# Kernel optimization log

Measured on AMD Instinct MI355X. Metric: run time of the kernel, lower is better.

Reference implementation:

```python
import jax, jax.numpy as jnp
import numpy as np

GAMMA = 0.002


def setup_inputs() -> dict:
    key = jax.random.key(0)
    k1, k2, k3, k4 = jax.random.split(key, 4)
    n, m, d = 16384, 8192, 512
    X = jax.random.normal(k1, (n, d), dtype=jnp.float32)
    Y = jax.random.normal(k2, (m, d), dtype=jnp.float32)
    # nn.Linear(m, 1): weight (1, m), bias (1,), default torch init ~ U(-1/sqrt(m), 1/sqrt(m))
    bound = 1.0 / np.sqrt(m)
    W = jax.random.uniform(k3, (1, m), dtype=jnp.float32, minval=-bound, maxval=bound)
    b = jax.random.uniform(k4, (1,), dtype=jnp.float32, minval=-bound, maxval=bound)
    return {"X": X, "Y": Y, "W": W, "b": b}


def reference(X, Y, W, b):
    # RBF Gram matrix via the GEMM squared-distance trick:
    x2 = jnp.sum(X * X, axis=-1, keepdims=True)          # (n, 1)
    y2 = jnp.sum(Y * Y, axis=-1)[None, :]                # (1, m)
    xy = jnp.einsum('nd,md->nm', X, Y)                   # (n, m)
    sq = jnp.maximum(x2 + y2 - 2.0 * xy, 0.0)            # clamp tiny negatives
    K = jnp.exp(-GAMMA * sq)                             # (n, m)
    # Linear(m -> 1) then squeeze(-1)
    out = jnp.einsum('nm,om->no', K, W) + b              # (n, 1)
    return out[:, 0]
```

## Files before the change

kernel.cpp:

```cpp
#include <hip/hip_runtime.h>
#include <hip/hip_bf16.h>


#define GAMMA 0.002f

typedef __bf16 bf16x8 __attribute__((ext_vector_type(8)));
typedef float  f32x4  __attribute__((ext_vector_type(4)));
typedef __attribute__((address_space(3))) void lds_void_t;
typedef __attribute__((address_space(1))) const void gl_void_t;

__global__ __launch_bounds__(256) void prep_x(const float* __restrict__ src,
                                              __bf16* __restrict__ dst,
                                              float* __restrict__ fac) {
    const int wid  = threadIdx.x >> 6;
    const int lane = threadIdx.x & 63;
    const int row  = blockIdx.x * 4 + wid;
    const float4* s = reinterpret_cast<const float4*>(src + (size_t)row * 512);
    float4 v0 = s[lane * 2];
    float4 v1 = s[lane * 2 + 1];
    float acc = v0.x * v0.x + v0.y * v0.y + v0.z * v0.z + v0.w * v0.w
              + v1.x * v1.x + v1.y * v1.y + v1.z * v1.z + v1.w * v1.w;
    bf16x8 o;
    o[0] = (__bf16)v0.x; o[1] = (__bf16)v0.y; o[2] = (__bf16)v0.z; o[3] = (__bf16)v0.w;
    o[4] = (__bf16)v1.x; o[5] = (__bf16)v1.y; o[6] = (__bf16)v1.z; o[7] = (__bf16)v1.w;
    *reinterpret_cast<bf16x8*>(dst + (size_t)row * 512 + lane * 8) = o;
#pragma unroll
    for (int off = 32; off >= 1; off >>= 1) acc += __shfl_xor(acc, off, 64);
    if (lane == 0) fac[row] = __expf(-GAMMA * acc);
}

__global__ __launch_bounds__(256) void prep_y(const float* __restrict__ src,
                                              __bf16* __restrict__ dst,
                                              float* __restrict__ fac,
                                              const float* __restrict__ W) {
    const int wid  = threadIdx.x >> 6;
    const int lane = threadIdx.x & 63;
    const int m    = blockIdx.x * 4 + wid;
    const float4* s = reinterpret_cast<const float4*>(src + (size_t)m * 512);
    float4 v0 = s[lane * 2];
    float4 v1 = s[lane * 2 + 1];
    float acc = v0.x * v0.x + v0.y * v0.y + v0.z * v0.z + v0.w * v0.w
              + v1.x * v1.x + v1.y * v1.y + v1.z * v1.z + v1.w * v1.w;
    bf16x8 o;
    o[0] = (__bf16)v0.x; o[1] = (__bf16)v0.y; o[2] = (__bf16)v0.z; o[3] = (__bf16)v0.w;
    o[4] = (__bf16)v1.x; o[5] = (__bf16)v1.y; o[6] = (__bf16)v1.z; o[7] = (__bf16)v1.w;
    const size_t idx = ((size_t)(lane >> 2) * 512 + (m >> 4)) * 512
                     + ((lane & 3) * 16 + (m & 15)) * 8;
    *reinterpret_cast<bf16x8*>(dst + idx) = o;
#pragma unroll
    for (int off = 32; off >= 1; off >>= 1) acc += __shfl_xor(acc, off, 64);
    if (lane == 0) fac[m] = __expf(-GAMMA * acc) * W[m];
}

__global__ void init_out(float* __restrict__ out, const float* __restrict__ b, int n) {
    int i = blockIdx.x * blockDim.x + threadIdx.x;
    if (i < n) out[i] = b[0];
}


#define LOADB(B, C) do { \
    const int q_ = (C) & 15, p_ = (C) >> 4; \
    const __bf16* bp_ = Ybt + ((size_t)q_ * 512 + cbgBase + p_ * 32) * 512 + lane8; \
    B[0] = *reinterpret_cast<const bf16x8*>(bp_); \
    B[1] = *reinterpret_cast<const bf16x8*>(bp_ + 512); \
    B[2] = *reinterpret_cast<const bf16x8*>(bp_ + 1024); \
    B[3] = *reinterpret_cast<const bf16x8*>(bp_ + 1536); \
} while (0)

#define READA(A, Q) do { \
    _Pragma("unroll") \
    for (int rb = 0; rb < 4; ++rb) \
        A[rb] = *reinterpret_cast<const bf16x8*>( \
            &smem[(Q) * 4096 + rb * 1024 + lane16]); \
} while (0)

#define MFMA16(A, B) do { \
    __builtin_amdgcn_s_setprio(1); \
    _Pragma("unroll") \
    for (int rb = 0; rb < 4; ++rb) \
        _Pragma("unroll") \
        for (int cb = 0; cb < 4; ++cb) \
            acc[rb][cb] = __builtin_amdgcn_mfma_f32_16x16x32_bf16( \
                A[rb], B[cb], acc[rb][cb], 0, 0, 0); \
    __builtin_amdgcn_s_setprio(0); \
} while (0)

__global__ __launch_bounds__(512, 4) void rbf_gemm(
    const __bf16* __restrict__ Xb, const __bf16* __restrict__ Ybt,
    const float* __restrict__ ex, const float* __restrict__ cwp,
    float* __restrict__ out) {
    __shared__ __align__(128) char smem[81920];

    const int tid  = threadIdx.x;
    const int wid  = tid >> 6;
    const int lane = tid & 63;

    const int pid = blockIdx.x;
    const int xcd = pid & 7;
    const int j   = pid >> 3;
    const int ch  = xcd & 1;
    const int rg  = (xcd >> 1) * 64 + j;
    const int rowBase = rg * 64;
    const int colBase = ch * 4096;
    const int cbgBase = ch * 256 + wid * 4;

    const int l15 = lane & 15, l4 = lane >> 4;
    const int lane16 = lane * 16;
    const int lane8  = lane * 8;

#pragma unroll
    for (int i = 0; i < 8; ++i) {
        const int blk = wid * 8 + i;
        const int q = blk >> 2, rb = blk & 3;
        const __bf16* src = Xb + (size_t)(rowBase + rb * 16 + l15) * 512 + q * 32 + l4 * 8;
        __builtin_amdgcn_global_load_lds((gl_void_t*)src,
            (lds_void_t*)(smem + q * 4096 + rb * 1024), 16, 0, 0);
    }
#pragma unroll
    for (int i = 0; i < 2; ++i)
        __builtin_amdgcn_global_load_lds(
            (gl_void_t*)(cwp + colBase + wid * 512 + i * 256 + lane * 4),
            (lds_void_t*)(smem + 65536 + wid * 2048 + i * 1024), 16, 0, 0);
    asm volatile("s_waitcnt vmcnt(0)");
    __builtin_amdgcn_s_barrier();

    f32x4 acc[4][4] = {};
    float rowsum[4][4] = {};

    bf16x8 A0[4], A1[4], B0[4], B1[4];
    LOADB(B0, 0);

    for (int cc = 0; cc < 64; ++cc) {
        const int ce = 2 * cc, co = 2 * cc + 1;
        LOADB(B1, co);
        READA(A0, ce & 15);
        MFMA16(A0, B0);
        LOADB(B0, (co + 1) & 127);
        READA(A1, co & 15);
        MFMA16(A1, B1);
        if ((cc & 7) == 7) {
            const int p = cc >> 3;
            float cv[4];
#pragma unroll
            for (int cb = 0; cb < 4; ++cb)
                cv[cb] = *reinterpret_cast<const float*>(
                    &smem[65536 + (p * 512 + wid * 64 + cb * 16 + l15) * 4]);
#pragma unroll
            for (int rb = 0; rb < 4; ++rb)
#pragma unroll
                for (int i2 = 0; i2 < 4; ++i2) {
                    float s = rowsum[rb][i2];
#pragma unroll
                    for (int cb = 0; cb < 4; ++cb)
                        s += __expf(0.004f * acc[rb][cb][i2]) * cv[cb];
                    rowsum[rb][i2] = s;
                }
#pragma unroll
            for (int rb = 0; rb < 4; ++rb)
#pragma unroll
                for (int cb = 0; cb < 4; ++cb)
                    acc[rb][cb] = (f32x4){0.f, 0.f, 0.f, 0.f};
        }
    }

#pragma unroll
    for (int rb = 0; rb < 4; ++rb)
#pragma unroll
        for (int i2 = 0; i2 < 4; ++i2) {
            float s = rowsum[rb][i2];
#pragma unroll
            for (int off = 1; off < 16; off <<= 1) s += __shfl_xor(s, off, 64);
            if (l15 == 0) {
                const int n = rowBase + rb * 16 + l4 * 4 + i2;
                atomicAdd(&out[n], ex[n] * s);
            }
        }
}

extern "C" void kernel_launch(void* const* d_in, const int* in_sizes, int n_in,
                              void* d_out, int out_size, void* d_ws, size_t ws_size,
                              hipStream_t stream) {
    const float* X = (const float*)d_in[0];
    const float* Y = (const float*)d_in[1];
    const float* W = (const float*)d_in[2];
    const float* b = (const float*)d_in[3];
    float* out = (float*)d_out;

    char* ws = (char*)d_ws;
    __bf16* Xb  = (__bf16*)(ws);
    __bf16* Ybt = (__bf16*)(ws + 16777216);
    float*  ex  = (float*)(ws + 16777216 + 8388608);
    float*  cw  = (float*)(ws + 16777216 + 8388608 + 65536);

    prep_x<<<4096, 256, 0, stream>>>(X, Xb, ex);
    prep_y<<<2048, 256, 0, stream>>>(Y, Ybt, cw, W);
    init_out<<<64, 256, 0, stream>>>(out, b, 16384);
    rbf_gemm<<<512, 512, 0, stream>>>(Xb, Ybt, ex, cw, out);
}
```

Measured before the change: 152.4 us.

## Fold output init into prep_x and drop B register double-buffering

The separate init_out launch is removed and the bias is written to out from prep_x's lane 0, saving one kernel launch. The GEMM main loop's manual double-buffered B loads (load the next chunk while computing the current one) are replaced by a single-buffer loop that loads B, reads A and then issues the MFMAs. This cuts register pressure but exposes global-load latency unless the compiler reschedules the loads, so the loop may stall more.

Result: faster. 145.4 us (-4.6%).

```diff
diff --git a/kernel.cpp b/kernel.cpp
--- a/kernel.cpp
+++ b/kernel.cpp
@@ -11,7 +11,9 @@
 
 __global__ __launch_bounds__(256) void prep_x(const float* __restrict__ src,
                                               __bf16* __restrict__ dst,
-                                              float* __restrict__ fac) {
+                                              float* __restrict__ fac,
+                                              float* __restrict__ out,
+                                              const float* __restrict__ bias) {
     const int wid  = threadIdx.x >> 6;
     const int lane = threadIdx.x & 63;
     const int row  = blockIdx.x * 4 + wid;
@@ -26,7 +28,10 @@
     *reinterpret_cast<bf16x8*>(dst + (size_t)row * 512 + lane * 8) = o;
 #pragma unroll
     for (int off = 32; off >= 1; off >>= 1) acc += __shfl_xor(acc, off, 64);
-    if (lane == 0) fac[row] = __expf(-GAMMA * acc);
+    if (lane == 0) {
+        fac[row] = __expf(-GAMMA * acc);
+        out[row] = bias[0];
+    }
 }
 
 __global__ __launch_bounds__(256) void prep_y(const float* __restrict__ src,
@@ -50,11 +55,6 @@
 #pragma unroll
     for (int off = 32; off >= 1; off >>= 1) acc += __shfl_xor(acc, off, 64);
     if (lane == 0) fac[m] = __expf(-GAMMA * acc) * W[m];
-}
-
-__global__ void init_out(float* __restrict__ out, const float* __restrict__ b, int n) {
-    int i = blockIdx.x * blockDim.x + threadIdx.x;
-    if (i < n) out[i] = b[0];
 }
 
 
@@ -127,19 +127,14 @@
     f32x4 acc[4][4] = {};
     float rowsum[4][4] = {};
 
-    bf16x8 A0[4], A1[4], B0[4], B1[4];
-    LOADB(B0, 0);
+    bf16x8 A[4], B[4];
 
-    for (int cc = 0; cc < 64; ++cc) {
-        const int ce = 2 * cc, co = 2 * cc + 1;
-        LOADB(B1, co);
-        READA(A0, ce & 15);
-        MFMA16(A0, B0);
-        LOADB(B0, (co + 1) & 127);
-        READA(A1, co & 15);
-        MFMA16(A1, B1);
-        if ((cc & 7) == 7) {
-            const int p = cc >> 3;
+    for (int c = 0; c < 128; ++c) {
+        LOADB(B, c);
+        READA(A, c & 15);
+        MFMA16(A, B);
+        if ((c & 15) == 15) {
+            const int p = c >> 4;
             float cv[4];
 #pragma unroll
             for (int cb = 0; cb < 4; ++cb)
@@ -192,8 +187,7 @@
     float*  ex  = (float*)(ws + 16777216 + 8388608);
     float*  cw  = (float*)(ws + 16777216 + 8388608 + 65536);
 
-    prep_x<<<4096, 256, 0, stream>>>(X, Xb, ex);
+    prep_x<<<4096, 256, 0, stream>>>(X, Xb, ex, out, b);
     prep_y<<<2048, 256, 0, stream>>>(Y, Ybt, cw, W);
-    init_out<<<64, 256, 0, stream>>>(out, b, 16384);
     rbf_gemm<<<512, 512, 0, stream>>>(Xb, Ybt, ex, cw, out);
 }
```
